# Performance work log

Measured on AMD Instinct MI355X. Metric: run time of the kernel, lower is better.

## Reference

```python
import jax, jax.numpy as jnp
import numpy as np

B, T, IN, H, OUT = 256, 512, 8, 128, 3


def setup_inputs() -> dict:
    key = jax.random.key(0)
    ks = jax.random.split(key, 16)
    s = 1.0 / np.sqrt(H)  # PyTorch LSTM init bound

    def u(k, shape):
        return jax.random.uniform(k, shape, jnp.float32, -s, s)

    inp = {"x": jax.random.normal(ks[0], (B, T, IN), jnp.float32)}
    ins = [IN, H, H]
    i = 1
    for l in range(3):
        inp[f"Wih{l}"] = u(ks[i], (4 * H, ins[l]))
        inp[f"Whh{l}"] = u(ks[i + 1], (4 * H, H))
        inp[f"bih{l}"] = u(ks[i + 2], (4 * H,))
        inp[f"bhh{l}"] = u(ks[i + 3], (4 * H,))
        i += 4
    inp["Wfc"] = u(ks[13], (OUT, H))
    inp["bfc"] = u(ks[14], (OUT,))
    return inp


def _lstm_layer(x, Wih, Whh, bih, bhh):
    # x: [T, B, in] -> (all hidden states [T, B, H], final hidden [B, H])
    # Precompute input contribution for every timestep (one big GEMM).
    xg = jnp.einsum('tbi,gi->tbg', x, Wih) + (bih + bhh)  # [T, B, 4H]

    def step(carry, xg_t):
        h, c = carry
        gates = xg_t + h @ Whh.T  # [B, 4H]
        i_, f_, g_, o_ = jnp.split(gates, 4, axis=-1)  # PyTorch gate order i,f,g,o
        c = jax.nn.sigmoid(f_) * c + jax.nn.sigmoid(i_) * jnp.tanh(g_)
        h = jax.nn.sigmoid(o_) * jnp.tanh(c)
        return (h, c), h

    h0 = jnp.zeros((x.shape[1], Whh.shape[1]), x.dtype)
    (hT, _), hs = jax.lax.scan(step, (h0, h0), xg)
    return hs, hT


def reference(x, Wih0, Whh0, bih0, bhh0, Wih1, Whh1, bih1, bhh1,
              Wih2, Whh2, bih2, bhh2, Wfc, bfc):
    xt = jnp.swapaxes(x, 0, 1)  # [T, B, IN]
    h1, _ = _lstm_layer(xt, Wih0, Whh0, bih0, bhh0)
    h2, _ = _lstm_layer(h1, Wih1, Whh1, bih1, bhh1)
    _, hT = _lstm_layer(h2, Wih2, Whh2, bih2, bhh2)  # only last step needed
    return hT @ Wfc.T + bfc  # [B, OUT]
```

## Files before the change

### kernel.cpp

```cpp
#include <hip/hip_runtime.h>

#define Bsz 256
#define Tt  512
#define Hh  128

#define OFF_WTHH 196608
#define OFF_BIAS 393216
#define OFF_HBUF 394752
#define OFF_FLAG 1181184
#define FLAG_N   6144

#define SKG(k) ((((k) >> 3) * 12) + ((k) & 7))

typedef unsigned long long u64;
typedef unsigned int u32;

__device__ __forceinline__ void st_h_agent(u64* p, float v, u32 seq) {
    u64 u = ((u64)seq << 32) | (u64)__float_as_uint(v);
    __hip_atomic_store(p, u, __ATOMIC_RELAXED, __HIP_MEMORY_SCOPE_AGENT);
}
__device__ __forceinline__ u64 ld_u64_agent(const u64* p) {
    return __hip_atomic_load(p, __ATOMIC_RELAXED, __HIP_MEMORY_SCOPE_AGENT);
}

__device__ __forceinline__ float4 stage4(const u64* __restrict__ src, u32 exp) {
    u64 a, b, c, d;
    for (;;) {
        a = ld_u64_agent(src + 0);
        b = ld_u64_agent(src + 1);
        c = ld_u64_agent(src + 2);
        d = ld_u64_agent(src + 3);
        if ((u32)(a >> 32) == exp && (u32)(b >> 32) == exp &&
            (u32)(c >> 32) == exp && (u32)(d >> 32) == exp) break;
    }
    return make_float4(__uint_as_float((u32)a), __uint_as_float((u32)b),
                       __uint_as_float((u32)c), __uint_as_float((u32)d));
}

__device__ __forceinline__ float fast_tanh(float x) {
    float e = __expf(2.f * x);
    return 1.f - 2.f / (e + 1.f);
}

template<int N>
__device__ __forceinline__ float row_shr_add(float v) {
    int s = __builtin_amdgcn_update_dpp(0, __float_as_int(v), 0x110 + N, 0xF, 0xF, true);
    return v + __int_as_float(s);
}
__device__ __forceinline__ float4 red16(float4 s) {
    s.x = row_shr_add<1>(s.x); s.x = row_shr_add<2>(s.x); s.x = row_shr_add<4>(s.x); s.x = row_shr_add<8>(s.x);
    s.y = row_shr_add<1>(s.y); s.y = row_shr_add<2>(s.y); s.y = row_shr_add<4>(s.y); s.y = row_shr_add<8>(s.y);
    s.z = row_shr_add<1>(s.z); s.z = row_shr_add<2>(s.z); s.z = row_shr_add<4>(s.z); s.z = row_shr_add<8>(s.z);
    s.w = row_shr_add<1>(s.w); s.w = row_shr_add<2>(s.w); s.w = row_shr_add<4>(s.w); s.w = row_shr_add<8>(s.w);
    return s;
}

#define FMA4(S, A, W) { S.x = fmaf(A, W.x, S.x); S.y = fmaf(A, W.y, S.y); \
                        S.z = fmaf(A, W.z, S.z); S.w = fmaf(A, W.w, S.w); }

__global__ void prep_kernel(const float* Wih0, const float* Whh0, const float* bih0, const float* bhh0,
                            const float* Wih1, const float* Whh1, const float* bih1, const float* bhh1,
                            const float* Wih2, const float* Whh2, const float* bih2, const float* bhh2,
                            float* ws)
{
    int gid = blockIdx.x * blockDim.x + threadIdx.x;
    if (gid < FLAG_N) ((int*)(ws + OFF_FLAG))[gid] = -1;
    u64* hb = (u64*)(ws + OFF_HBUF);
    for (int i = gid; i < 4 * 3 * 256 * 128; i += 6144) hb[i] = 0xFFFFFFFF00000000ull;
    if (gid >= 3 * 512) return;
    int l = gid >> 9, gc = gid & 511;
    const float* Wih = (l == 0) ? Wih0 : (l == 1) ? Wih1 : Wih2;
    const float* Whh = (l == 0) ? Whh0 : (l == 1) ? Whh1 : Whh2;
    const float* bih = (l == 0) ? bih0 : (l == 1) ? bih1 : bih2;
    const float* bhh = (l == 0) ? bhh0 : (l == 1) ? bhh1 : bhh2;
    int Kin = (l == 0) ? 8 : 128;
    float* Wt_ih = ws + (size_t)l * 128 * 512;
    float* Wt_hh = ws + OFF_WTHH + (size_t)l * 128 * 512;
    float* bias  = ws + OFF_BIAS + l * 512;
    for (int k = 0; k < 128; k++) Wt_ih[k * 512 + gc] = (k < Kin) ? Wih[gc * Kin + k] : 0.f;
    for (int k = 0; k < 128; k++) Wt_hh[k * 512 + gc] = Whh[gc * 128 + k];
    bias[gc] = bih[gc] + bhh[gc];
}

__global__ __launch_bounds__(512, 2) void lstm_kernel(const float* __restrict__ x,
                                                      float* __restrict__ ws)
{
    const float* __restrict__ bias = ws + OFF_BIAS;
    u64* __restrict__ hbuf = (u64*)(ws + OFF_HBUF);
    int* __restrict__ fl = (int*)(ws + OFF_FLAG);

    const int layer = blockIdx.x >> 6;
    const int tile  = blockIdx.x & 63;
    const int rt  = tile & 15;
    const int hct = tile >> 4;
    const int r0  = rt << 4;
    const int hc0 = hct << 5;
    const int tid = threadIdx.x;

    __shared__ float sAin[16][192];
    __shared__ float sArec[16][192];
    __shared__ float sG[16][132];

    for (int i = tid; i < 16 * 192; i += 512) ((float*)sAin)[i] = 0.f;

    int* adflag = nullptr;
    if (tid < 4)                    adflag = fl + ((layer * 16 + rt) * 4 + tid) * 32;
    else if (tid < 8 && layer < 2)  adflag = fl + (((layer + 1) * 16 + rt) * 4 + (tid - 4)) * 32;
    int* myflag = fl + ((layer * 16 + rt) * 4 + hct) * 32;

    const int kg = tid & 15;
    const int rg = (tid >> 4) & 1;
    const int cg = tid >> 5;
    const int cbase = cg << 3;
    const int gcb = ((cbase >> 5) << 7) + hc0 + (cbase & 31);
    const int ka = kg * 12;

    const float* Wl_ih = ws + (size_t)layer * 65536;
    const float* Wl_hh = ws + OFF_WTHH + (size_t)layer * 65536;
    float4 wihA[8], wihB[8], whhA[8], whhB[8];
#pragma unroll
    for (int kk = 0; kk < 8; kk++) {
        int k = kg * 8 + kk;
        wihA[kk] = *(const float4*)&Wl_ih[(size_t)k * 512 + gcb];
        wihB[kk] = *(const float4*)&Wl_ih[(size_t)k * 512 + gcb + 4];
        whhA[kk] = *(const float4*)&Wl_hh[(size_t)k * 512 + gcb];
        whhB[kk] = *(const float4*)&Wl_hh[(size_t)k * 512 + gcb + 4];
    }
    float4 bias4a = *(const float4*)&bias[layer * 512 + gcb];
    float4 bias4b = *(const float4*)&bias[layer * 512 + gcb + 4];
    if (kg != 15) {
        bias4a = make_float4(0.f, 0.f, 0.f, 0.f);
        bias4b = make_float4(0.f, 0.f, 0.f, 0.f);
    }

    const int sr = tid >> 5;
    const int sk = (tid & 31) << 2;
    const int skc = SKG(sk);

    const int ur = tid >> 5, uc = tid & 31;
    float creg = 0.f;

    __syncthreads();

    for (int t = 0; t < Tt; ++t) {
        const int s = t + layer;
        const int prev = (s - 1) & 3, cur = s & 3;
        const u32 expseq = (u32)(s - 1);

        if (layer == 0) {
            if (tid < 128) {
                int r = tid >> 3, i = tid & 7;
                sAin[r][i] = x[((size_t)(r0 + r) * Tt + t) * 8 + i];
            }
            if (t > 0) {
                const u64* src = hbuf + ((size_t)prev * 3 + layer) * Bsz * Hh
                               + (size_t)(r0 + sr) * Hh + sk;
                *(float4*)&sArec[sr][skc] = stage4(src, expseq);
            }
        } else {
            const u64* srcA = hbuf + ((size_t)prev * 3 + (layer - 1)) * Bsz * Hh
                            + (size_t)(r0 + sr) * Hh + sk;
            if (t > 0) {
                const u64* srcR = hbuf + ((size_t)prev * 3 + layer) * Bsz * Hh
                                + (size_t)(r0 + sr) * Hh + sk;
                u64 a0, a1, a2, a3, b0, b1, b2, b3;
                for (;;) {
                    a0 = ld_u64_agent(srcA + 0); a1 = ld_u64_agent(srcA + 1);
                    a2 = ld_u64_agent(srcA + 2); a3 = ld_u64_agent(srcA + 3);
                    b0 = ld_u64_agent(srcR + 0); b1 = ld_u64_agent(srcR + 1);
                    b2 = ld_u64_agent(srcR + 2); b3 = ld_u64_agent(srcR + 3);
                    if ((u32)(a0 >> 32) == expseq && (u32)(a1 >> 32) == expseq &&
                        (u32)(a2 >> 32) == expseq && (u32)(a3 >> 32) == expseq &&
                        (u32)(b0 >> 32) == expseq && (u32)(b1 >> 32) == expseq &&
                        (u32)(b2 >> 32) == expseq && (u32)(b3 >> 32) == expseq) break;
                }
                *(float4*)&sAin[sr][skc]  = make_float4(__uint_as_float((u32)a0), __uint_as_float((u32)a1),
                                                        __uint_as_float((u32)a2), __uint_as_float((u32)a3));
                *(float4*)&sArec[sr][skc] = make_float4(__uint_as_float((u32)b0), __uint_as_float((u32)b1),
                                                        __uint_as_float((u32)b2), __uint_as_float((u32)b3));
            } else {
                *(float4*)&sAin[sr][skc] = stage4(srcA, expseq);
            }
        }
        __syncthreads();

        if (tid == 0)
            __hip_atomic_store(myflag, s, __ATOMIC_RELAXED, __HIP_MEMORY_SCOPE_AGENT);

        if (adflag != nullptr) {
            const int target = s - 3;
            while (__hip_atomic_load(adflag, __ATOMIC_RELAXED, __HIP_MEMORY_SCOPE_AGENT) < target)
                __builtin_amdgcn_s_sleep(1);
        }

#pragma unroll
        for (int j = 0; j < 8; j++) {
            const int r = rg * 8 + j;
            float4 acc0 = bias4a, acc1 = bias4b;
            {
                float4 a0 = *(const float4*)&sAin[r][ka];
                float4 a1 = *(const float4*)&sAin[r][ka + 4];
                FMA4(acc0, a0.x, wihA[0]); FMA4(acc1, a0.x, wihB[0]);
                FMA4(acc0, a0.y, wihA[1]); FMA4(acc1, a0.y, wihB[1]);
                FMA4(acc0, a0.z, wihA[2]); FMA4(acc1, a0.z, wihB[2]);
                FMA4(acc0, a0.w, wihA[3]); FMA4(acc1, a0.w, wihB[3]);
                FMA4(acc0, a1.x, wihA[4]); FMA4(acc1, a1.x, wihB[4]);
                FMA4(acc0, a1.y, wihA[5]); FMA4(acc1, a1.y, wihB[5]);
                FMA4(acc0, a1.z, wihA[6]); FMA4(acc1, a1.z, wihB[6]);
                FMA4(acc0, a1.w, wihA[7]); FMA4(acc1, a1.w, wihB[7]);
            }
            if (t > 0) {
                float4 b0 = *(const float4*)&sArec[r][ka];
                float4 b1 = *(const float4*)&sArec[r][ka + 4];
                FMA4(acc0, b0.x, whhA[0]); FMA4(acc1, b0.x, whhB[0]);
                FMA4(acc0, b0.y, whhA[1]); FMA4(acc1, b0.y, whhB[1]);
                FMA4(acc0, b0.z, whhA[2]); FMA4(acc1, b0.z, whhB[2]);
                FMA4(acc0, b0.w, whhA[3]); FMA4(acc1, b0.w, whhB[3]);
                FMA4(acc0, b1.x, whhA[4]); FMA4(acc1, b1.x, whhB[4]);
                FMA4(acc0, b1.y, whhA[5]); FMA4(acc1, b1.y, whhB[5]);
                FMA4(acc0, b1.z, whhA[6]); FMA4(acc1, b1.z, whhB[6]);
                FMA4(acc0, b1.w, whhA[7]); FMA4(acc1, b1.w, whhB[7]);
            }
            acc0 = red16(acc0);
            acc1 = red16(acc1);
            if (kg == 15) {
                *(float4*)&sG[r][cbase]     = acc0;
                *(float4*)&sG[r][cbase + 4] = acc1;
            }
        }
        __syncthreads();

        {
            float gi = sG[ur][uc],      gf = sG[ur][32 + uc];
            float gg = sG[ur][64 + uc], go = sG[ur][96 + uc];
            float si = 1.f / (1.f + __expf(-gi));
            float sf = 1.f / (1.f + __expf(-gf));
            float so = 1.f / (1.f + __expf(-go));
            creg = sf * creg + si * fast_tanh(gg);
            u64* dst = hbuf + ((size_t)cur * 3 + layer) * Bsz * Hh
                     + (size_t)(r0 + ur) * Hh + hc0 + uc;
            st_h_agent(dst, so * fast_tanh(creg), (u32)s);
        }
    }
}

__global__ void fc_kernel(const float* __restrict__ ws, const float* __restrict__ Wfc,
                          const float* __restrict__ bfc, float* __restrict__ out)
{
    const u64* h2 = (const u64*)(ws + OFF_HBUF) + (size_t)(1 * 3 + 2) * Bsz * Hh;
    int b = threadIdx.x;
    float a0 = bfc[0], a1 = bfc[1], a2 = bfc[2];
    for (int k = 0; k < 128; k++) {
        float h = __uint_as_float((u32)h2[b * 128 + k]);
        a0 += h * Wfc[0 * 128 + k];
        a1 += h * Wfc[1 * 128 + k];
        a2 += h * Wfc[2 * 128 + k];
    }
    out[b * 3 + 0] = a0;
    out[b * 3 + 1] = a1;
    out[b * 3 + 2] = a2;
}

extern "C" void kernel_launch(void* const* d_in, const int* in_sizes, int n_in,
                              void* d_out, int out_size, void* d_ws, size_t ws_size,
                              hipStream_t stream)
{
    const float* x = (const float*)d_in[0];
    float* ws = (float*)d_ws;

    prep_kernel<<<24, 256, 0, stream>>>(
        (const float*)d_in[1],  (const float*)d_in[2],  (const float*)d_in[3],  (const float*)d_in[4],
        (const float*)d_in[5],  (const float*)d_in[6],  (const float*)d_in[7],  (const float*)d_in[8],
        (const float*)d_in[9],  (const float*)d_in[10], (const float*)d_in[11], (const float*)d_in[12],
        ws);

    void* args[2] = { (void*)&x, (void*)&ws };
    hipLaunchCooperativeKernel((void*)lstm_kernel, dim3(192), dim3(512), args, 0, stream);

    fc_kernel<<<1, 256, 0, stream>>>(ws, (const float*)d_in[13], (const float*)d_in[14], (float*)d_out);
}
```

Measured before the change: 3.283 ms.

## Overlap input-projection FMAs with the recurrent-state spin wait

```diff
diff --git a/kernel.cpp b/kernel.cpp
--- a/kernel.cpp
+++ b/kernel.cpp
@@ -147,40 +147,53 @@
         const int prev = (s - 1) & 3, cur = s & 3;
         const u32 expseq = (u32)(s - 1);
 
+        const u64* srcR = hbuf + ((size_t)prev * 3 + layer) * Bsz * Hh
+                        + (size_t)(r0 + sr) * Hh + sk;
+        u64 b0 = 0, b1 = 0, b2 = 0, b3 = 0;
+        if (t > 0) {
+            b0 = ld_u64_agent(srcR + 0); b1 = ld_u64_agent(srcR + 1);
+            b2 = ld_u64_agent(srcR + 2); b3 = ld_u64_agent(srcR + 3);
+        }
+
         if (layer == 0) {
             if (tid < 128) {
                 int r = tid >> 3, i = tid & 7;
                 sAin[r][i] = x[((size_t)(r0 + r) * Tt + t) * 8 + i];
             }
-            if (t > 0) {
-                const u64* src = hbuf + ((size_t)prev * 3 + layer) * Bsz * Hh
-                               + (size_t)(r0 + sr) * Hh + sk;
-                *(float4*)&sArec[sr][skc] = stage4(src, expseq);
-            }
         } else {
             const u64* srcA = hbuf + ((size_t)prev * 3 + (layer - 1)) * Bsz * Hh
                             + (size_t)(r0 + sr) * Hh + sk;
-            if (t > 0) {
-                const u64* srcR = hbuf + ((size_t)prev * 3 + layer) * Bsz * Hh
-                                + (size_t)(r0 + sr) * Hh + sk;
-                u64 a0, a1, a2, a3, b0, b1, b2, b3;
-                for (;;) {
-                    a0 = ld_u64_agent(srcA + 0); a1 = ld_u64_agent(srcA + 1);
-                    a2 = ld_u64_agent(srcA + 2); a3 = ld_u64_agent(srcA + 3);
-                    b0 = ld_u64_agent(srcR + 0); b1 = ld_u64_agent(srcR + 1);
-                    b2 = ld_u64_agent(srcR + 2); b3 = ld_u64_agent(srcR + 3);
-                    if ((u32)(a0 >> 32) == expseq && (u32)(a1 >> 32) == expseq &&
-                        (u32)(a2 >> 32) == expseq && (u32)(a3 >> 32) == expseq &&
-                        (u32)(b0 >> 32) == expseq && (u32)(b1 >> 32) == expseq &&
-                        (u32)(b2 >> 32) == expseq && (u32)(b3 >> 32) == expseq) break;
-                }
-                *(float4*)&sAin[sr][skc]  = make_float4(__uint_as_float((u32)a0), __uint_as_float((u32)a1),
-                                                        __uint_as_float((u32)a2), __uint_as_float((u32)a3));
-                *(float4*)&sArec[sr][skc] = make_float4(__uint_as_float((u32)b0), __uint_as_float((u32)b1),
-                                                        __uint_as_float((u32)b2), __uint_as_float((u32)b3));
-            } else {
-                *(float4*)&sAin[sr][skc] = stage4(srcA, expseq);
-            }
+            *(float4*)&sAin[sr][skc] = stage4(srcA, expseq);
+        }
+        __syncthreads();
+
+        float4 acc[8][2];
+#pragma unroll
+        for (int j = 0; j < 8; j++) { acc[j][0] = bias4a; acc[j][1] = bias4b; }
+#pragma unroll
+        for (int j = 0; j < 8; j++) {
+            const int r = rg * 8 + j;
+            float4 a0 = *(const float4*)&sAin[r][ka];
+            float4 a1 = *(const float4*)&sAin[r][ka + 4];
+            FMA4(acc[j][0], a0.x, wihA[0]); FMA4(acc[j][1], a0.x, wihB[0]);
+            FMA4(acc[j][0], a0.y, wihA[1]); FMA4(acc[j][1], a0.y, wihB[1]);
+            FMA4(acc[j][0], a0.z, wihA[2]); FMA4(acc[j][1], a0.z, wihB[2]);
+            FMA4(acc[j][0], a0.w, wihA[3]); FMA4(acc[j][1], a0.w, wihB[3]);
+            FMA4(acc[j][0], a1.x, wihA[4]); FMA4(acc[j][1], a1.x, wihB[4]);
+            FMA4(acc[j][0], a1.y, wihA[5]); FMA4(acc[j][1], a1.y, wihB[5]);
+            FMA4(acc[j][0], a1.z, wihA[6]); FMA4(acc[j][1], a1.z, wihB[6]);
+            FMA4(acc[j][0], a1.w, wihA[7]); FMA4(acc[j][1], a1.w, wihB[7]);
+        }
+
+        if (t > 0) {
+            while ((u32)(b0 >> 32) != expseq || (u32)(b1 >> 32) != expseq ||
+                   (u32)(b2 >> 32) != expseq || (u32)(b3 >> 32) != expseq) {
+                b0 = ld_u64_agent(srcR + 0); b1 = ld_u64_agent(srcR + 1);
+                b2 = ld_u64_agent(srcR + 2); b3 = ld_u64_agent(srcR + 3);
+            }
+            *(float4*)&sArec[sr][skc] = make_float4(
+                __uint_as_float((u32)b0), __uint_as_float((u32)b1),
+                __uint_as_float((u32)b2), __uint_as_float((u32)b3));
         }
         __syncthreads();
 
@@ -193,39 +206,30 @@
                 __builtin_amdgcn_s_sleep(1);
         }
 
+        if (t > 0) {
+#pragma unroll
+            for (int j = 0; j < 8; j++) {
+                const int r = rg * 8 + j;
+                float4 c0 = *(const float4*)&sArec[r][ka];
+                float4 c1 = *(const float4*)&sArec[r][ka + 4];
+                FMA4(acc[j][0], c0.x, whhA[0]); FMA4(acc[j][1], c0.x, whhB[0]);
+                FMA4(acc[j][0], c0.y, whhA[1]); FMA4(acc[j][1], c0.y, whhB[1]);
+                FMA4(acc[j][0], c0.z, whhA[2]); FMA4(acc[j][1], c0.z, whhB[2]);
+                FMA4(acc[j][0], c0.w, whhA[3]); FMA4(acc[j][1], c0.w, whhB[3]);
+                FMA4(acc[j][0], c1.x, whhA[4]); FMA4(acc[j][1], c1.x, whhB[4]);
+                FMA4(acc[j][0], c1.y, whhA[5]); FMA4(acc[j][1], c1.y, whhB[5]);
+                FMA4(acc[j][0], c1.z, whhA[6]); FMA4(acc[j][1], c1.z, whhB[6]);
+                FMA4(acc[j][0], c1.w, whhA[7]); FMA4(acc[j][1], c1.w, whhB[7]);
+            }
+        }
+
 #pragma unroll
         for (int j = 0; j < 8; j++) {
-            const int r = rg * 8 + j;
-            float4 acc0 = bias4a, acc1 = bias4b;
-            {
-                float4 a0 = *(const float4*)&sAin[r][ka];
-                float4 a1 = *(const float4*)&sAin[r][ka + 4];
-                FMA4(acc0, a0.x, wihA[0]); FMA4(acc1, a0.x, wihB[0]);
-                FMA4(acc0, a0.y, wihA[1]); FMA4(acc1, a0.y, wihB[1]);
-                FMA4(acc0, a0.z, wihA[2]); FMA4(acc1, a0.z, wihB[2]);
-                FMA4(acc0, a0.w, wihA[3]); FMA4(acc1, a0.w, wihB[3]);
-                FMA4(acc0, a1.x, wihA[4]); FMA4(acc1, a1.x, wihB[4]);
-                FMA4(acc0, a1.y, wihA[5]); FMA4(acc1, a1.y, wihB[5]);
-                FMA4(acc0, a1.z, wihA[6]); FMA4(acc1, a1.z, wihB[6]);
-                FMA4(acc0, a1.w, wihA[7]); FMA4(acc1, a1.w, wihB[7]);
-            }
-            if (t > 0) {
-                float4 b0 = *(const float4*)&sArec[r][ka];
-                float4 b1 = *(const float4*)&sArec[r][ka + 4];
-                FMA4(acc0, b0.x, whhA[0]); FMA4(acc1, b0.x, whhB[0]);
-                FMA4(acc0, b0.y, whhA[1]); FMA4(acc1, b0.y, whhB[1]);
-                FMA4(acc0, b0.z, whhA[2]); FMA4(acc1, b0.z, whhB[2]);
-                FMA4(acc0, b0.w, whhA[3]); FMA4(acc1, b0.w, whhB[3]);
-                FMA4(acc0, b1.x, whhA[4]); FMA4(acc1, b1.x, whhB[4]);
-                FMA4(acc0, b1.y, whhA[5]); FMA4(acc1, b1.y, whhB[5]);
-                FMA4(acc0, b1.z, whhA[6]); FMA4(acc1, b1.z, whhB[6]);
-                FMA4(acc0, b1.w, whhA[7]); FMA4(acc1, b1.w, whhB[7]);
-            }
-            acc0 = red16(acc0);
-            acc1 = red16(acc1);
+            float4 r0v = red16(acc[j][0]);
+            float4 r1v = red16(acc[j][1]);
             if (kg == 15) {
-                *(float4*)&sG[r][cbase]     = acc0;
-                *(float4*)&sG[r][cbase + 4] = acc1;
+                *(float4*)&sG[rg * 8 + j][cbase]     = r0v;
+                *(float4*)&sG[rg * 8 + j][cbase + 4] = r1v;
             }
         }
         __syncthreads();
```

New measurement: 3.383 ms. 3.0% more time.
